# Kernel tuning notes

Hardware: AMD Instinct MI355X
Metric: run time of the kernel (lower is better)

The kernel has to match this reference:

```python
import jax, jax.numpy as jnp
import numpy as np

# Model dims (see init_kwargs)
B, S, H = 1, 1024, 2048
NH, NKV, HD = 16, 4, 128       # query heads, kv heads (GQA), head dim
RD = 64                        # partial rotary dim
E, TOPK, I = 8, 2, 1024        # experts, top-k, expert intermediate
EPS = 1e-6
THETA = 1000000.0


def setup_inputs() -> dict:
    key = jax.random.key(0)
    ks = jax.random.split(key, 12)
    s = 0.02  # init scale
    return {
        "hidden_states": jax.random.normal(ks[0], (B, S, H), jnp.float32),
        "position_ids": jnp.tile(jnp.arange(S, dtype=jnp.int32), (B, 1)),
        "ln1_w": jnp.ones((H,), jnp.float32),
        "q_norm_w": jnp.ones((NH * HD,), jnp.float32),
        "k_norm_w": jnp.ones((NKV * HD,), jnp.float32),
        "wq": jax.random.normal(ks[1], (H, NH * HD), jnp.float32) * s,
        "wk": jax.random.normal(ks[2], (H, NKV * HD), jnp.float32) * s,
        "wv": jax.random.normal(ks[3], (H, NKV * HD), jnp.float32) * s,
        "wo": jax.random.normal(ks[4], (NH * HD, H), jnp.float32) * s,
        "ln2_w": jnp.ones((H,), jnp.float32),
        "router_w": jax.random.normal(ks[5], (H, E), jnp.float32) * s,
        "router_bias": jax.random.normal(ks[6], (E,), jnp.float32) * 0.1,
        "w_gate": jax.random.normal(ks[7], (E, H, I), jnp.float32) * s,
        "w_up": jax.random.normal(ks[8], (E, H, I), jnp.float32) * s,
        "w_down": jax.random.normal(ks[9], (E, I, H), jnp.float32) * s,
    }


def rmsnorm(x, w):
    # fp32 RMSNorm over full last dim (matches DistributedRMSNorm with tp=1)
    xf = x.astype(jnp.float32)
    r = jax.lax.rsqrt(jnp.mean(xf * xf, axis=-1, keepdims=True) + EPS)
    return (xf * r * w).astype(x.dtype)


def _rope(x, cos, sin):
    # partial rotary: only first RD dims of each head are rotated
    xr, xp = x[..., :RD], x[..., RD:]
    half = RD // 2
    rot = jnp.concatenate([-xr[..., half:], xr[..., :half]], axis=-1)
    return jnp.concatenate([xr * cos + rot * sin, xp], axis=-1)


def reference(hidden_states, position_ids, ln1_w, q_norm_w, k_norm_w,
              wq, wk, wv, wo, ln2_w, router_w, router_bias,
              w_gate, w_up, w_down):
    x = hidden_states
    # --- attention block ---
    h = rmsnorm(x, ln1_w)
    Q = h @ wq  # [B,S,NH*HD]
    K = h @ wk  # [B,S,NKV*HD]
    V = h @ wv
    # MiniMax M2 qk_norm: RMSNorm over FULL projection output BEFORE head reshape
    Q = rmsnorm(Q, q_norm_w)
    K = rmsnorm(K, k_norm_w)
    q = Q.reshape(B, S, NH, HD).transpose(0, 2, 1, 3)   # [B,NH,S,HD]
    k = K.reshape(B, S, NKV, HD).transpose(0, 2, 1, 3)  # [B,NKV,S,HD]
    v = V.reshape(B, S, NKV, HD).transpose(0, 2, 1, 3)
    # partial RoPE
    inv = 1.0 / (THETA ** (jnp.arange(0, RD, 2, dtype=jnp.float32) / RD))
    ang = position_ids.astype(jnp.float32)[:, :, None] * inv  # [B,S,RD/2]
    cos = jnp.concatenate([jnp.cos(ang)] * 2, axis=-1)[:, None]  # [B,1,S,RD]
    sin = jnp.concatenate([jnp.sin(ang)] * 2, axis=-1)[:, None]
    q = _rope(q, cos, sin)
    k = _rope(k, cos, sin)
    # GQA expand
    rep = NH // NKV
    k = jnp.repeat(k, rep, axis=1)
    v = jnp.repeat(v, rep, axis=1)
    scores = jnp.einsum('bhqd,bhkd->bhqk', q, k).astype(jnp.float32) / np.sqrt(HD).astype(np.float32)
    causal = jnp.tril(jnp.ones((S, S), bool))
    scores = jnp.where(causal, scores, jnp.float32(-1e30))
    attn = jax.nn.softmax(scores, axis=-1).astype(v.dtype)
    ctx = jnp.einsum('bhqk,bhkd->bhqd', attn, v)
    attn_out = ctx.transpose(0, 2, 1, 3).reshape(B, S, NH * HD) @ wo
    res = x + attn_out
    # --- MoE block ---
    h2 = rmsnorm(res, ln2_w)
    t = h2.reshape(B * S, H)
    logits = t.astype(jnp.float32) @ router_w        # [T,E]
    sc = jax.nn.sigmoid(logits)
    # top-k chosen on bias-corrected scores; weights from uncorrected scores
    _, ti = jax.lax.top_k(sc + router_bias, TOPK)    # [T,TOPK]
    aff = jnp.take_along_axis(sc, ti, axis=-1)
    aff = aff / jnp.sum(aff, axis=-1, keepdims=True)  # normalize_top_k_affinities
    T = B * S
    combine = jnp.zeros((T, E), jnp.float32).at[jnp.arange(T)[:, None], ti].add(aff)
    # SwiGLU experts (dense-compute, sparse-combine reference for blockwise grouped GEMM)
    g = jnp.einsum('th,ehi->tei', t, w_gate)
    u = jnp.einsum('th,ehi->tei', t, w_up)
    act = jax.nn.silu(g) * u
    eo = jnp.einsum('tei,eih->teh', act, w_down)
    moe = jnp.einsum('te,teh->th', combine.astype(eo.dtype), eo)
    return res + moe.reshape(B, S, H)
```

## Files before the change

### kernel.cpp

```cpp
#include <hip/hip_runtime.h>
#include <hip/hip_bf16.h>
#include <cstdint>

static constexpr int S   = 1024;
static constexpr int H   = 2048;
static constexpr int NH  = 16;
static constexpr int NKV = 4;
static constexpr int HD  = 128;
static constexpr int EXPN = 8;
static constexpr int FFI = 1024;

typedef __bf16 bf16x8 __attribute__((ext_vector_type(8)));
typedef float  f32x4  __attribute__((ext_vector_type(4)));
typedef unsigned short ushortx8 __attribute__((ext_vector_type(8)));

#define DEVI __device__ __forceinline__

DEVI unsigned short f2bf(float f) {
    union { float f; uint32_t u; } v; v.f = f;
    uint32_t r = (v.u + 0x7FFFu + ((v.u >> 16) & 1u)) >> 16;
    return (unsigned short)r;
}
DEVI float bf2f(unsigned short s) {
    union { uint32_t u; float f; } v; v.u = ((uint32_t)s) << 16; return v.f;
}

DEVI void atomAdd(float* p, float v) { unsafeAtomicAdd(p, v); }

__global__ __launch_bounds__(256) void transT(const float* __restrict__ in,
                                              unsigned short* __restrict__ outp,
                                              int R, int C)
{
    __shared__ unsigned short tl[64][72];
    int zb = blockIdx.z;
    in   += (size_t)zb * R * C;
    outp += (size_t)zb * R * C;
    int c0 = blockIdx.x * 64, r0 = blockIdx.y * 64;
    int t = threadIdx.x;
    int cq = (t & 15) * 4;
    int rr = t >> 4;
    #pragma unroll
    for (int p = 0; p < 4; ++p) {
        int row = rr + p * 16;
        float4 v = *(const float4*)&in[(size_t)(r0 + row) * C + c0 + cq];
        tl[cq + 0][row] = f2bf(v.x);
        tl[cq + 1][row] = f2bf(v.y);
        tl[cq + 2][row] = f2bf(v.z);
        tl[cq + 3][row] = f2bf(v.w);
    }
    __syncthreads();
    int r8 = (t & 7) * 8;
    int cc = t >> 3;
    #pragma unroll
    for (int p = 0; p < 2; ++p) {
        int col = cc + p * 32;
        ushortx8 v = *(const ushortx8*)&tl[col][r8];
        *(ushortx8*)&outp[(size_t)(c0 + col) * R + r0 + r8] = v;
    }
}

enum { CFG_PROJ3 = 0, CFG_WO = 1, CFG_SCORES = 2, CFG_PV = 3, CFG_GATEUP = 4, CFG_DOWN = 5 };

template<int CFG, int WM>
__global__ __launch_bounds__(256, 2) void gemm_k(
    const unsigned short* __restrict__ A,
    const unsigned short* __restrict__ B0,
    const unsigned short* __restrict__ B1,
    const unsigned short* __restrict__ B2,
    float* __restrict__ C0,
    float* __restrict__ C1,
    float* __restrict__ C2,
    unsigned short* __restrict__ Cb,
    const float* __restrict__ X,
    const int* __restrict__ cnt,
    const int* __restrict__ tokList,
    int arg0)
{
    constexpr bool DUAL = (CFG == CFG_GATEUP);
    constexpr int BM = WM * 32;

    const int tid = threadIdx.x;
    const int m0 = blockIdx.y * BM;
    int n0 = blockIdx.x * 128;

    int M = S;
    int kbeg = 0, kend = 0, LDA = 0, LDBK = 0, LDC = 0;
    const unsigned short* Ap = A;
    const unsigned short* Bb = B0;
    const unsigned short* Bb2 = B1;
    const int* tlist = nullptr;
    float* Cout = C0;
    int head = 0, e = 0, hl = 0;

    if constexpr (CFG == CFG_PROJ3) {
        int xt = blockIdx.x;
        if (xt < 16)      { Bb = B0; Cout = C0; LDC = 2048; n0 = xt * 128; }
        else if (xt < 20) { Bb = B1; Cout = C1; LDC = 512;  n0 = (xt - 16) * 128; }
        else              { Bb = B2; Cout = C2; LDC = 512;  n0 = (xt - 20) * 128; }
        LDA = H; LDBK = H; kend = H;
    } else if constexpr (CFG == CFG_WO) {
        LDA = H; LDBK = H; LDC = H; kend = H;
    } else if constexpr (CFG == CFG_SCORES) {
        hl = blockIdx.z; head = arg0 + hl;
        if (n0 >= m0 + BM) return;
        Ap = A + (size_t)head * S * HD;
        Bb = B0 + (size_t)(head >> 2) * S * HD;
        kend = HD; LDA = HD; LDBK = HD;
    } else if constexpr (CFG == CFG_PV) {
        int z = blockIdx.z; hl = z >> 2; int ks = z & 3;
        head = arg0 + hl;
        int kcap = m0 + BM;
        kbeg = ks * 256;
        if (kbeg >= kcap) return;
        kend = (kbeg + 256 < kcap) ? kbeg + 256 : kcap;
        Ap = A + (size_t)hl * S * S;
        Bb = B0 + (size_t)(head >> 2) * HD * S;
        LDA = S; LDBK = S;
    } else if constexpr (CFG == CFG_GATEUP) {
        e = blockIdx.z;
        M = cnt[e]; if (m0 >= M) return;
        tlist = tokList + e * S;
        Bb  = B0 + (size_t)e * FFI * H;
        Bb2 = B1 + (size_t)e * FFI * H;
        kend = H; LDA = H; LDBK = H;
    } else {
        e = blockIdx.z;
        M = cnt[e]; if (m0 >= M) return;
        Ap = A + (size_t)e * S * FFI;
        Bb = B0 + (size_t)e * H * FFI;
        kend = FFI; LDA = FFI; LDBK = FFI;
    }

    __shared__ unsigned short As[BM * 64];
    __shared__ unsigned short Bs[128 * 64];
    __shared__ unsigned short Bs2[DUAL ? 128 * 64 : 8];

    const int lane = tid & 63, grp = lane >> 4, r16 = lane & 15;
    const int wid = tid >> 6, wr = wid >> 1, wc = wid & 1;

    f32x4 acc[WM][4] = {};
    f32x4 acc2[DUAL ? WM : 1][DUAL ? 4 : 1] = {};

    for (int k0 = kbeg; k0 < kend; k0 += 64) {
        __syncthreads();
        #pragma unroll
        for (int i = 0; i < WM; ++i) {
            int chunk = tid + i * 256;
            int row = chunk >> 3;
            int kc  = (chunk & 7) * 8;
            int grow = m0 + row;
            if constexpr (CFG == CFG_GATEUP) { int r2 = grow < M ? grow : M - 1; grow = tlist[r2]; }
            else if constexpr (CFG == CFG_DOWN) { grow = grow < M ? grow : M - 1; }
            ushortx8 v = *(const ushortx8*)&Ap[(size_t)grow * LDA + k0 + kc];
            *(ushortx8*)&As[row * 64 + (kc ^ ((row & 7) << 3))] = v;
        }
        #pragma unroll
        for (int i = 0; i < 4; ++i) {
            int chunk = tid + i * 256;
            int row = chunk >> 3;
            int kc  = (chunk & 7) * 8;
            int idx = row * 64 + (kc ^ ((row & 7) << 3));
            ushortx8 v = *(const ushortx8*)&Bb[(size_t)(n0 + row) * LDBK + k0 + kc];
            *(ushortx8*)&Bs[idx] = v;
            if constexpr (DUAL) {
                ushortx8 v2 = *(const ushortx8*)&Bb2[(size_t)(n0 + row) * LDBK + k0 + kc];
                *(ushortx8*)&Bs2[idx] = v2;
            }
        }
        __syncthreads();
        #pragma unroll
        for (int kk = 0; kk < 64; kk += 32) {
            bf16x8 af[WM], bfr[4], bfr2[DUAL ? 4 : 1];
            #pragma unroll
            for (int mi = 0; mi < WM; ++mi) {
                int r = wr * (WM * 16) + mi * 16 + r16;
                int idx = r * 64 + ((kk + grp * 8) ^ ((r & 7) << 3));
                af[mi] = __builtin_bit_cast(bf16x8, *(const ushortx8*)&As[idx]);
            }
            #pragma unroll
            for (int ni = 0; ni < 4; ++ni) {
                int r = wc * 64 + ni * 16 + r16;
                int idx = r * 64 + ((kk + grp * 8) ^ ((r & 7) << 3));
                bfr[ni] = __builtin_bit_cast(bf16x8, *(const ushortx8*)&Bs[idx]);
                if constexpr (DUAL)
                    bfr2[ni] = __builtin_bit_cast(bf16x8, *(const ushortx8*)&Bs2[idx]);
            }
            #pragma unroll
            for (int mi = 0; mi < WM; ++mi)
                #pragma unroll
                for (int ni = 0; ni < 4; ++ni) {
                    acc[mi][ni] = __builtin_amdgcn_mfma_f32_16x16x32_bf16(af[mi], bfr[ni], acc[mi][ni], 0, 0, 0);
                    if constexpr (DUAL)
                        acc2[mi][ni] = __builtin_amdgcn_mfma_f32_16x16x32_bf16(af[mi], bfr2[ni], acc2[mi][ni], 0, 0, 0);
                }
        }
    }

    #pragma unroll
    for (int mi = 0; mi < WM; ++mi) {
        #pragma unroll
        for (int ni = 0; ni < 4; ++ni) {
            f32x4 v = acc[mi][ni];
            int col = n0 + wc * 64 + ni * 16 + r16;
            #pragma unroll
            for (int j = 0; j < 4; ++j) {
                int row = m0 + wr * (WM * 16) + mi * 16 + grp * 4 + j;
                float val = v[j];
                if constexpr (CFG == CFG_PROJ3) {
                    Cout[(size_t)row * LDC + col] = val;
                } else if constexpr (CFG == CFG_WO) {
                    C0[(size_t)row * H + col] = val + X[(size_t)row * H + col];
                } else if constexpr (CFG == CFG_SCORES) {
                    float sv = val * 0.08838834764831845f;
                    if (col > row) sv = -1e30f;
                    C0[((size_t)hl * S + row) * S + col] = sv;
                } else if constexpr (CFG == CFG_PV) {
                    atomAdd(&C0[(size_t)row * 2048 + head * HD + col], val);
                } else if constexpr (CFG == CFG_GATEUP) {
                    if (row < M) {
                        float g = val, u = acc2[mi][ni][j];
                        float a = g / (1.f + expf(-g)) * u;
                        Cb[((size_t)e * S + row) * FFI + col] = f2bf(a);
                    }
                } else {
                    if (row < M) {
                        Cb[((size_t)e * S + row) * H + col] = f2bf(val);
                    }
                }
            }
        }
    }
}

__global__ __launch_bounds__(256) void rms_h(const float* __restrict__ x,
                                             const float* __restrict__ w,
                                             unsigned short* __restrict__ out)
{
    int row = blockIdx.x, tid = threadIdx.x;
    const float* xr = x + (size_t)row * H;
    float4 a = *(const float4*)&xr[tid * 8];
    float4 b = *(const float4*)&xr[tid * 8 + 4];
    float vals[8] = { a.x, a.y, a.z, a.w, b.x, b.y, b.z, b.w };
    float ss = 0;
    #pragma unroll
    for (int j = 0; j < 8; ++j) ss += vals[j] * vals[j];
    __shared__ float red[4];
    #pragma unroll
    for (int o = 32; o; o >>= 1) ss += __shfl_down(ss, o);
    if ((tid & 63) == 0) red[tid >> 6] = ss;
    __syncthreads();
    float tot = red[0] + red[1] + red[2] + red[3];
    float r = rsqrtf(tot * (1.f / H) + 1e-6f);
    ushortx8 ov;
    #pragma unroll
    for (int j = 0; j < 8; ++j) ov[j] = f2bf(vals[j] * r * w[tid * 8 + j]);
    *(ushortx8*)&out[(size_t)row * H + tid * 8] = ov;
}

__global__ __launch_bounds__(256) void qnorm_rope(const float* __restrict__ qbuf,
                                                  const float* __restrict__ qw,
                                                  const int* __restrict__ pos,
                                                  unsigned short* __restrict__ qatt)
{
    int tok = blockIdx.x, tid = threadIdx.x;
    __shared__ float sh[2048];
    __shared__ float red[4];
    const float* xr = qbuf + (size_t)tok * 2048;
    float4 a = *(const float4*)&xr[tid * 8];
    float4 b = *(const float4*)&xr[tid * 8 + 4];
    *(float4*)&sh[tid * 8] = a;
    *(float4*)&sh[tid * 8 + 4] = b;
    float ss = a.x*a.x + a.y*a.y + a.z*a.z + a.w*a.w + b.x*b.x + b.y*b.y + b.z*b.z + b.w*b.w;
    #pragma unroll
    for (int o = 32; o; o >>= 1) ss += __shfl_down(ss, o);
    if ((tid & 63) == 0) red[tid >> 6] = ss;
    __syncthreads();
    float tot = red[0] + red[1] + red[2] + red[3];
    float r = rsqrtf(tot * (1.f / 2048.f) + 1e-6f);
    float p = (float)pos[tok];
    #pragma unroll
    for (int j = 0; j < 8; ++j) {
        int idx = tid * 8 + j;
        int d = idx & 127, hh = idx >> 7;
        float v = sh[idx] * r * qw[idx];
        float o;
        if (d < 64) {
            int jj = d & 31;
            float ang = p * expf((float)jj * -0.43173470268f);
            float c = cosf(ang), sn = sinf(ang);
            if (d < 32) { float v2 = sh[idx + 32] * r * qw[idx + 32]; o = v * c - v2 * sn; }
            else        { float v2 = sh[idx - 32] * r * qw[idx - 32]; o = v * c + v2 * sn; }
        } else o = v;
        qatt[((size_t)hh * S + tok) * HD + d] = f2bf(o);
    }
}

__global__ __launch_bounds__(256) void knorm_rope(const float* __restrict__ kbuf,
                                                  const float* __restrict__ kw,
                                                  const int* __restrict__ pos,
                                                  unsigned short* __restrict__ katt)
{
    int tok = blockIdx.x, tid = threadIdx.x;
    __shared__ float sh[512];
    __shared__ float red[4];
    const float* xr = kbuf + (size_t)tok * 512;
    float2 a = *(const float2*)&xr[tid * 2];
    sh[tid * 2] = a.x; sh[tid * 2 + 1] = a.y;
    float ss = a.x * a.x + a.y * a.y;
    #pragma unroll
    for (int o = 32; o; o >>= 1) ss += __shfl_down(ss, o);
    if ((tid & 63) == 0) red[tid >> 6] = ss;
    __syncthreads();
    float tot = red[0] + red[1] + red[2] + red[3];
    float r = rsqrtf(tot * (1.f / 512.f) + 1e-6f);
    float p = (float)pos[tok];
    #pragma unroll
    for (int j = 0; j < 2; ++j) {
        int idx = tid * 2 + j;
        int d = idx & 127, hh = idx >> 7;
        float v = sh[idx] * r * kw[idx];
        float o;
        if (d < 64) {
            int jj = d & 31;
            float ang = p * expf((float)jj * -0.43173470268f);
            float c = cosf(ang), sn = sinf(ang);
            if (d < 32) { float v2 = sh[idx + 32] * r * kw[idx + 32]; o = v * c - v2 * sn; }
            else        { float v2 = sh[idx - 32] * r * kw[idx - 32]; o = v * c + v2 * sn; }
        } else o = v;
        katt[((size_t)hh * S + tok) * HD + d] = f2bf(o);
    }
}

__global__ __launch_bounds__(256) void softmax_k(const float* __restrict__ scores,
                                                 unsigned short* __restrict__ pb)
{
    int bid = blockIdx.x;
    int hl = bid >> 10, q = bid & 1023;
    const float* srow = scores + ((size_t)hl * S + q) * S;
    unsigned short* prow = pb + ((size_t)hl * S + q) * S;
    int L = q + 1, tid = threadIdx.x;
    __shared__ float red[4];
    float v[4]; float mx = -3.4e38f;
    #pragma unroll
    for (int i = 0; i < 4; ++i) {
        int j = tid + i * 256;
        if (j < L) { v[i] = srow[j]; mx = fmaxf(mx, v[i]); } else v[i] = 0.f;
    }
    float m = mx;
    #pragma unroll
    for (int o = 32; o; o >>= 1) m = fmaxf(m, __shfl_down(m, o));
    if ((tid & 63) == 0) red[tid >> 6] = m;
    __syncthreads();
    float M_ = fmaxf(fmaxf(red[0], red[1]), fmaxf(red[2], red[3]));
    __syncthreads();
    float e[4]; float sum = 0;
    #pragma unroll
    for (int i = 0; i < 4; ++i) {
        int j = tid + i * 256;
        if (j < L) { e[i] = expf(v[i] - M_); sum += e[i]; } else e[i] = 0.f;
    }
    #pragma unroll
    for (int o = 32; o; o >>= 1) sum += __shfl_down(sum, o);
    if ((tid & 63) == 0) red[tid >> 6] = sum;
    __syncthreads();
    float inv = 1.f / (red[0] + red[1] + red[2] + red[3]);
    #pragma unroll
    for (int i = 0; i < 4; ++i) {
        int j = tid + i * 256;
        prow[j] = f2bf(e[i] * inv);
    }
}

__global__ void zero_cnt(int* cnt) { if (threadIdx.x < EXPN) cnt[threadIdx.x] = 0; }

__global__ void zerok(float4* __restrict__ p, int n4)
{
    int i = blockIdx.x * 256 + threadIdx.x;
    if (i < n4) p[i] = float4{0.f, 0.f, 0.f, 0.f};
}

__global__ void cvt_k(const float* __restrict__ src, unsigned short* __restrict__ dst)
{
    int i = blockIdx.x * 256 + threadIdx.x;
    float4 a = *(const float4*)&src[i * 8];
    float4 b = *(const float4*)&src[i * 8 + 4];
    float v[8] = { a.x, a.y, a.z, a.w, b.x, b.y, b.z, b.w };
    ushortx8 o;
    #pragma unroll
    for (int j = 0; j < 8; ++j) o[j] = f2bf(v[j]);
    *(ushortx8*)&dst[i * 8] = o;
}

__global__ __launch_bounds__(256) void router_k(const float* __restrict__ res,
                                                const float* __restrict__ ln2w,
                                                const float* __restrict__ rw,
                                                const float* __restrict__ rbias,
                                                int* __restrict__ cnt,
                                                int* __restrict__ tokList,
                                                int* __restrict__ slot,
                                                float* __restrict__ slotw)
{
    int tok = blockIdx.x, tid = threadIdx.x;
    const float* xr = res + (size_t)tok * H;
    float4 a = *(const float4*)&xr[tid * 8];
    float4 b = *(const float4*)&xr[tid * 8 + 4];
    float vals[8] = { a.x, a.y, a.z, a.w, b.x, b.y, b.z, b.w };
    float ss = 0;
    #pragma unroll
    for (int j = 0; j < 8; ++j) ss += vals[j] * vals[j];
    __shared__ float red[4];
    float t_ = ss;
    #pragma unroll
    for (int o = 32; o; o >>= 1) t_ += __shfl_down(t_, o);
    if ((tid & 63) == 0) red[tid >> 6] = t_;
    __syncthreads();
    float tot = red[0] + red[1] + red[2] + red[3];
    float r = rsqrtf(tot * (1.f / H) + 1e-6f);

    float acc[EXPN] = {};
    #pragma unroll
    for (int j = 0; j < 8; ++j) {
        float tv = vals[j] * r * ln2w[tid * 8 + j];
        const float* rp = rw + (size_t)(tid * 8 + j) * EXPN;
        #pragma unroll
        for (int e = 0; e < EXPN; ++e) acc[e] += tv * rp[e];
    }
    __shared__ float r8[4][EXPN];
    #pragma unroll
    for (int e = 0; e < EXPN; ++e) {
        float s_ = acc[e];
        #pragma unroll
        for (int o = 32; o; o >>= 1) s_ += __shfl_down(s_, o);
        acc[e] = s_;
    }
    if ((tid & 63) == 0)
        for (int e = 0; e < EXPN; ++e) r8[tid >> 6][e] = acc[e];
    __syncthreads();
    if (tid == 0) {
        float sg[EXPN];
        for (int e = 0; e < EXPN; ++e) {
            float lg = r8[0][e] + r8[1][e] + r8[2][e] + r8[3][e];
            sg[e] = 1.f / (1.f + expf(-lg));
        }
        int i0 = 0; float b0 = -1e30f;
        for (int e = 0; e < EXPN; ++e) {
            float s_ = sg[e] + rbias[e];
            if (s_ > b0) { b0 = s_; i0 = e; }
        }
        int i1 = -1; float b1 = -1e30f;
        for (int e = 0; e < EXPN; ++e) {
            if (e == i0) continue;
            float s_ = sg[e] + rbias[e];
            if (s_ > b1) { b1 = s_; i1 = e; }
        }
        float a0 = sg[i0], a1 = sg[i1], inv = 1.f / (a0 + a1);
        int p0 = atomicAdd(&cnt[i0], 1);
        tokList[i0 * S + p0] = tok;
        int p1 = atomicAdd(&cnt[i1], 1);
        tokList[i1 * S + p1] = tok;
        slot[tok * 2]     = i0 * S + p0;  slotw[tok * 2]     = a0 * inv;
        slot[tok * 2 + 1] = i1 * S + p1;  slotw[tok * 2 + 1] = a1 * inv;
    }
}

__global__ __launch_bounds__(256) void combine_k(const unsigned short* __restrict__ eo,
                                                 const int* __restrict__ slot,
                                                 const float* __restrict__ slotw,
                                                 float* __restrict__ out)
{
    int t = blockIdx.x;
    int c = threadIdx.x * 8;
    int s0 = slot[t * 2], s1 = slot[t * 2 + 1];
    float w0 = slotw[t * 2], w1 = slotw[t * 2 + 1];
    ushortx8 a = *(const ushortx8*)&eo[(size_t)s0 * H + c];
    ushortx8 b = *(const ushortx8*)&eo[(size_t)s1 * H + c];
    size_t base = (size_t)t * H + c;
    float4 o0 = *(float4*)&out[base];
    float4 o1 = *(float4*)&out[base + 4];
    float ov[8] = { o0.x, o0.y, o0.z, o0.w, o1.x, o1.y, o1.z, o1.w };
    #pragma unroll
    for (int j = 0; j < 8; ++j)
        ov[j] += w0 * bf2f(a[j]) + w1 * bf2f(b[j]);
    *(float4*)&out[base]     = float4{ ov[0], ov[1], ov[2], ov[3] };
    *(float4*)&out[base + 4] = float4{ ov[4], ov[5], ov[6], ov[7] };
}

extern "C" void kernel_launch(void* const* d_in, const int* in_sizes, int n_in,
                              void* d_out, int out_size, void* d_ws, size_t ws_size,
                              hipStream_t stream)
{
    const float* x     = (const float*)d_in[0];
    const int*   pos   = (const int*)d_in[1];
    const float* ln1w  = (const float*)d_in[2];
    const float* qnw   = (const float*)d_in[3];
    const float* knw   = (const float*)d_in[4];
    const float* wq    = (const float*)d_in[5];
    const float* wk    = (const float*)d_in[6];
    const float* wv    = (const float*)d_in[7];
    const float* wo    = (const float*)d_in[8];
    const float* ln2w  = (const float*)d_in[9];
    const float* rw    = (const float*)d_in[10];
    const float* rbias = (const float*)d_in[11];
    const float* wg    = (const float*)d_in[12];
    const float* wu    = (const float*)d_in[13];
    const float* wd    = (const float*)d_in[14];
    float* out = (float*)d_out;

    char* ws = (char*)d_ws;
    const size_t MB = 1024 * 1024;
    unsigned short* h_bf = (unsigned short*)(ws + 0);
    float* qbuf  = (float*)(ws + 4 * MB);
    float* ctxf  = (float*)(ws + 4 * MB);
    float* kbuf  = (float*)(ws + 12 * MB);
    float* vbuf  = (float*)(ws + 14 * MB);
    unsigned short* qatt = (unsigned short*)(ws + 16 * MB);
    unsigned short* katt = (unsigned short*)(ws + 20 * MB);
    unsigned short* vT   = (unsigned short*)(ws + 21 * MB);
    unsigned short* ctx  = (unsigned short*)(ws + 22 * MB);
    unsigned short* tbf  = (unsigned short*)(ws + 26 * MB);
    int*   cnt     = (int*)(ws + 30 * MB);
    int*   tokList = (int*)(ws + 30 * MB + 4096);
    int*   slot    = (int*)(ws + 30 * MB + 512 * 1024);
    float* slotw   = (float*)(ws + 30 * MB + 768 * 1024);
    float* scores = (float*)(ws + 31 * MB);
    unsigned short* pbuf = (unsigned short*)(ws + 63 * MB);
    unsigned short* act = (unsigned short*)(ws + 31 * MB);
    unsigned short* eo  = (unsigned short*)(ws + 47 * MB);
    unsigned short* wqT = (unsigned short*)(ws + 79 * MB);
    unsigned short* wkT = (unsigned short*)(ws + 87 * MB);
    unsigned short* wvT = (unsigned short*)(ws + 89 * MB);
    unsigned short* woT = (unsigned short*)(ws + 91 * MB);
    unsigned short* wgT = (unsigned short*)(ws + 99 * MB);
    unsigned short* wuT = (unsigned short*)(ws + 131 * MB);
    unsigned short* wdT = (unsigned short*)(ws + 163 * MB);

    transT<<<dim3(32, 32, 1), 256, 0, stream>>>(wq, wqT, 2048, 2048);
    transT<<<dim3(8,  32, 1), 256, 0, stream>>>(wk, wkT, 2048, 512);
    transT<<<dim3(8,  32, 1), 256, 0, stream>>>(wv, wvT, 2048, 512);
    transT<<<dim3(32, 32, 1), 256, 0, stream>>>(wo, woT, 2048, 2048);
    transT<<<dim3(16, 32, 8), 256, 0, stream>>>(wg, wgT, 2048, 1024);
    transT<<<dim3(16, 32, 8), 256, 0, stream>>>(wu, wuT, 2048, 1024);
    transT<<<dim3(32, 16, 8), 256, 0, stream>>>(wd, wdT, 1024, 2048);

    rms_h<<<S, 256, 0, stream>>>(x, ln1w, h_bf);

    gemm_k<CFG_PROJ3, 2><<<dim3(24, 16, 1), 256, 0, stream>>>(h_bf, wqT, wkT, wvT, qbuf, kbuf, vbuf, nullptr, nullptr, nullptr, nullptr, 0);

    qnorm_rope<<<S, 256, 0, stream>>>(qbuf, qnw, pos, qatt);
    knorm_rope<<<S, 256, 0, stream>>>(kbuf, knw, pos, katt);
    transT<<<dim3(8, 16, 1), 256, 0, stream>>>(vbuf, vT, 1024, 512);
    zerok<<<2048, 256, 0, stream>>>((float4*)ctxf, (8 * MB) / 16);

    for (int hc = 0; hc < 2; ++hc) {
        gemm_k<CFG_SCORES, 4><<<dim3(8, 8, 8), 256, 0, stream>>>(qatt, katt, nullptr, nullptr, scores, nullptr, nullptr, nullptr, nullptr, nullptr, nullptr, hc * 8);
        softmax_k<<<8 * S, 256, 0, stream>>>(scores, pbuf);
        gemm_k<CFG_PV, 4><<<dim3(1, 8, 32), 256, 0, stream>>>(pbuf, vT, nullptr, nullptr, ctxf, nullptr, nullptr, nullptr, nullptr, nullptr, nullptr, hc * 8);
    }
    cvt_k<<<(S * 2048) / (256 * 8), 256, 0, stream>>>(ctxf, ctx);

    gemm_k<CFG_WO, 2><<<dim3(16, 16, 1), 256, 0, stream>>>(ctx, woT, nullptr, nullptr, out, nullptr, nullptr, nullptr, x, nullptr, nullptr, 0);

    rms_h<<<S, 256, 0, stream>>>(out, ln2w, tbf);
    zero_cnt<<<1, 64, 0, stream>>>(cnt);
    router_k<<<S, 256, 0, stream>>>(out, ln2w, rw, rbias, cnt, tokList, slot, slotw);

    gemm_k<CFG_GATEUP, 2><<<dim3(8, 16, EXPN), 256, 0, stream>>>(tbf, wgT, wuT, nullptr, nullptr, nullptr, nullptr, act, nullptr, cnt, tokList, 0);
    gemm_k<CFG_DOWN, 2><<<dim3(16, 16, EXPN), 256, 0, stream>>>(act, wdT, nullptr, nullptr, nullptr, nullptr, nullptr, eo, nullptr, cnt, tokList, 0);
    combine_k<<<S, 256, 0, stream>>>(eo, slot, slotw, out);
}
```

Before: 398.6 us.

## Double-buffer GEMM tiles with direct global-to-LDS loads

The shared GEMM kernel now stages A and B tiles straight from global memory into LDS with global_load_lds, instead of going through registers. The swizzle moves to the global-address side, and the per-row offsets (including the token-list gather) are computed once before the K loop. LDS is double-buffered, so the next K tile is prefetched while MFMAs run on the current one, with one barrier per iteration. The cost is twice the LDS per block, which may lower occupancy, mostly for the dual gate/up configuration.

```diff
diff --git a/kernel.cpp b/kernel.cpp
--- a/kernel.cpp
+++ b/kernel.cpp
@@ -26,6 +26,13 @@
 }
 
 DEVI void atomAdd(float* p, float v) { unsafeAtomicAdd(p, v); }
+
+DEVI void gll16(const unsigned short* g, unsigned short* l) {
+    __builtin_amdgcn_global_load_lds(
+        (const __attribute__((address_space(1))) unsigned int*)(g),
+        (__attribute__((address_space(3))) unsigned int*)(l),
+        16, 0, 0);
+}
 
 __global__ __launch_bounds__(256) void transT(const float* __restrict__ in,
                                               unsigned short* __restrict__ outp,
@@ -78,6 +85,8 @@
 {
     constexpr bool DUAL = (CFG == CFG_GATEUP);
     constexpr int BM = WM * 32;
+    constexpr int ASZ = BM * 64;
+    constexpr int BSZ = 128 * 64;
 
     const int tid = threadIdx.x;
     const int m0 = blockIdx.y * BM;
@@ -131,56 +140,70 @@
         kend = FFI; LDA = FFI; LDBK = FFI;
     }
 
-    __shared__ unsigned short As[BM * 64];
-    __shared__ unsigned short Bs[128 * 64];
-    __shared__ unsigned short Bs2[DUAL ? 128 * 64 : 8];
+    __shared__ unsigned short As[2 * ASZ];
+    __shared__ unsigned short Bs[2 * BSZ];
+    __shared__ unsigned short Bs2[DUAL ? 2 * BSZ : 8];
 
     const int lane = tid & 63, grp = lane >> 4, r16 = lane & 15;
     const int wid = tid >> 6, wr = wid >> 1, wc = wid & 1;
+    const int wbase8 = (tid & 0xFFC0) * 8;
+
+    size_t aoff[WM];
+    #pragma unroll
+    for (int c = 0; c < WM; ++c) {
+        int chunk = c * 256 + tid;
+        int row = chunk >> 3;
+        int kcs = (chunk & 7) * 8;
+        int grow = m0 + row;
+        if constexpr (CFG == CFG_GATEUP) { int r2 = grow < M ? grow : M - 1; grow = tlist[r2]; }
+        else if constexpr (CFG == CFG_DOWN) { grow = grow < M ? grow : M - 1; }
+        aoff[c] = (size_t)grow * LDA + (kcs ^ ((row & 7) << 3));
+    }
+    size_t boff[4];
+    #pragma unroll
+    for (int c = 0; c < 4; ++c) {
+        int chunk = c * 256 + tid;
+        int row = chunk >> 3;
+        int kcs = (chunk & 7) * 8;
+        boff[c] = (size_t)(n0 + row) * LDBK + (kcs ^ ((row & 7) << 3));
+    }
+
+    auto STAGE = [&](int buf, int k0) {
+        #pragma unroll
+        for (int c = 0; c < WM; ++c)
+            gll16(Ap + aoff[c] + k0, &As[buf * ASZ + c * 2048 + wbase8]);
+        #pragma unroll
+        for (int c = 0; c < 4; ++c)
+            gll16(Bb + boff[c] + k0, &Bs[buf * BSZ + c * 2048 + wbase8]);
+        if constexpr (DUAL) {
+            #pragma unroll
+            for (int c = 0; c < 4; ++c)
+                gll16(Bb2 + boff[c] + k0, &Bs2[buf * BSZ + c * 2048 + wbase8]);
+        }
+    };
 
     f32x4 acc[WM][4] = {};
     f32x4 acc2[DUAL ? WM : 1][DUAL ? 4 : 1] = {};
 
+    int cur = 0;
+    STAGE(0, kbeg);
+    __syncthreads();
+
     for (int k0 = kbeg; k0 < kend; k0 += 64) {
-        __syncthreads();
-        #pragma unroll
-        for (int i = 0; i < WM; ++i) {
-            int chunk = tid + i * 256;
-            int row = chunk >> 3;
-            int kc  = (chunk & 7) * 8;
-            int grow = m0 + row;
-            if constexpr (CFG == CFG_GATEUP) { int r2 = grow < M ? grow : M - 1; grow = tlist[r2]; }
-            else if constexpr (CFG == CFG_DOWN) { grow = grow < M ? grow : M - 1; }
-            ushortx8 v = *(const ushortx8*)&Ap[(size_t)grow * LDA + k0 + kc];
-            *(ushortx8*)&As[row * 64 + (kc ^ ((row & 7) << 3))] = v;
-        }
-        #pragma unroll
-        for (int i = 0; i < 4; ++i) {
-            int chunk = tid + i * 256;
-            int row = chunk >> 3;
-            int kc  = (chunk & 7) * 8;
-            int idx = row * 64 + (kc ^ ((row & 7) << 3));
-            ushortx8 v = *(const ushortx8*)&Bb[(size_t)(n0 + row) * LDBK + k0 + kc];
-            *(ushortx8*)&Bs[idx] = v;
-            if constexpr (DUAL) {
-                ushortx8 v2 = *(const ushortx8*)&Bb2[(size_t)(n0 + row) * LDBK + k0 + kc];
-                *(ushortx8*)&Bs2[idx] = v2;
-            }
-        }
-        __syncthreads();
+        if (k0 + 64 < kend) STAGE(cur ^ 1, k0 + 64);
         #pragma unroll
         for (int kk = 0; kk < 64; kk += 32) {
             bf16x8 af[WM], bfr[4], bfr2[DUAL ? 4 : 1];
             #pragma unroll
             for (int mi = 0; mi < WM; ++mi) {
                 int r = wr * (WM * 16) + mi * 16 + r16;
-                int idx = r * 64 + ((kk + grp * 8) ^ ((r & 7) << 3));
+                int idx = cur * ASZ + r * 64 + ((kk + grp * 8) ^ ((r & 7) << 3));
                 af[mi] = __builtin_bit_cast(bf16x8, *(const ushortx8*)&As[idx]);
             }
             #pragma unroll
             for (int ni = 0; ni < 4; ++ni) {
                 int r = wc * 64 + ni * 16 + r16;
-                int idx = r * 64 + ((kk + grp * 8) ^ ((r & 7) << 3));
+                int idx = cur * BSZ + r * 64 + ((kk + grp * 8) ^ ((r & 7) << 3));
                 bfr[ni] = __builtin_bit_cast(bf16x8, *(const ushortx8*)&Bs[idx]);
                 if constexpr (DUAL)
                     bfr2[ni] = __builtin_bit_cast(bf16x8, *(const ushortx8*)&Bs2[idx]);
@@ -194,6 +217,8 @@
                         acc2[mi][ni] = __builtin_amdgcn_mfma_f32_16x16x32_bf16(af[mi], bfr2[ni], acc2[mi][ni], 0, 0, 0);
                 }
         }
+        __syncthreads();
+        cur ^= 1;
     }
 
     #pragma unroll
```

New measurement: 381.2 us. 1.05x faster.
